# Kernel tuning notes

Hardware: AMD Instinct MI355X
Metric: run time of the kernel (lower is better)

## Reference

```python
import jax, jax.numpy as jnp
import numpy as np

K = 3
PAD = 1
KK = K * K
GROUPS = 32  # min(32, dim) with dim=64
EPS = 1e-5


def _conv(x, w, pad):
    return jax.lax.conv_general_dilated(
        x, w, (1, 1), [(pad, pad), (pad, pad)],
        dimension_numbers=('NCHW', 'OIHW', 'NCHW'))


def _bilinear_gather(x, py, px):
    # x: (B,C,H,W); py,px: (B,KK,H,W) float sampling coords (zero pad outside)
    B, C, H, W = x.shape
    xf = x.reshape(B, C, H * W)
    y0f = jnp.floor(py)
    x0f = jnp.floor(px)
    wy1 = py - y0f  # fractional weights (differentiable path to offsets)
    wx1 = px - x0f
    y0 = y0f.astype(jnp.int32)
    x0 = x0f.astype(jnp.int32)

    def g(yi, xi):
        valid = (yi >= 0) & (yi < H) & (xi >= 0) & (xi < W)
        idx = (jnp.clip(yi, 0, H - 1) * W + jnp.clip(xi, 0, W - 1)).reshape(B, 1, -1)
        v = jnp.take_along_axis(xf, idx, axis=2).reshape(B, C, KK, H, W)
        return v * valid[:, None].astype(x.dtype)

    v00 = g(y0, x0)
    v01 = g(y0, x0 + 1)
    v10 = g(y0 + 1, x0)
    v11 = g(y0 + 1, x0 + 1)
    wy1e = wy1[:, None]
    wx1e = wx1[:, None]
    return (v00 * (1 - wy1e) * (1 - wx1e) + v01 * (1 - wy1e) * wx1e
            + v10 * wy1e * (1 - wx1e) + v11 * wy1e * wx1e)


def _forward(x, w_off1, w_off2, w_mask1, w_mask2, weight, bias, gamma, beta):
    B, C, H, W = x.shape
    # offset branch: 1x1 conv then KxK conv -> (B, 2*KK, H, W)
    off = _conv(_conv(x, w_off1, 0), w_off2, PAD).reshape(B, KK, 2, H, W)
    # mask branch -> sigmoid modulation (B, KK, H, W)
    mask = jax.nn.sigmoid(_conv(_conv(x, w_mask1, 0), w_mask2, PAD))
    # base kernel grid (torchvision deform_conv2d: pairs are (dy, dx) per tap)
    ky = jnp.repeat(jnp.arange(K) - PAD, K).astype(x.dtype)
    kx = jnp.tile(jnp.arange(K) - PAD, K).astype(x.dtype)
    py = off[:, :, 0] + jnp.arange(H, dtype=x.dtype)[None, None, :, None] + ky[None, :, None, None]
    px = off[:, :, 1] + jnp.arange(W, dtype=x.dtype)[None, None, None, :] + kx[None, :, None, None]
    samp = _bilinear_gather(x, py, px)  # (B, C, KK, H, W)
    # depthwise deformable conv: per-channel weight over KK taps, modulated by mask
    out = jnp.einsum('bkhw,ck,bckhw->bchw', mask, weight.reshape(C, KK), samp)
    out = out + bias[None, :, None, None]
    # GroupNorm(32, C)
    g = out.reshape(B, GROUPS, C // GROUPS, H, W)
    mu = g.mean(axis=(2, 3, 4), keepdims=True)
    var = g.var(axis=(2, 3, 4), keepdims=True)
    gn = ((g - mu) * jax.lax.rsqrt(var + EPS)).reshape(B, C, H, W)
    gn = gn * gamma[None, :, None, None] + beta[None, :, None, None]
    return jax.nn.gelu(gn, approximate=False)


def setup_inputs() -> dict:
    key = jax.random.key(0)
    ks = jax.random.split(key, 6)
    B, C, H, W = 4, 64, 128, 128
    x = jax.random.normal(ks[0], (B, C, H, W), dtype=jnp.float32)
    w_off1 = jax.random.normal(ks[1], (C, C, 1, 1), dtype=jnp.float32) * 0.05
    w_off2 = jax.random.normal(ks[2], (2 * KK, C, K, K), dtype=jnp.float32) * 0.02
    w_mask1 = jax.random.normal(ks[3], (C, C, 1, 1), dtype=jnp.float32) * 0.05
    w_mask2 = jax.random.normal(ks[4], (KK, C, K, K), dtype=jnp.float32) * 0.05
    bound = 1.0 / np.sqrt(KK)  # kaiming_uniform(a=1) for (C,1,K,K) -> fan_in=KK
    weight = jax.random.uniform(ks[5], (C, 1, K, K), dtype=jnp.float32,
                                minval=-bound, maxval=bound)
    bias = jnp.zeros((C,), dtype=jnp.float32)
    gamma = jnp.ones((C,), dtype=jnp.float32)
    beta = jnp.zeros((C,), dtype=jnp.float32)
    return {'x': x, 'w_off1': w_off1, 'w_off2': w_off2, 'w_mask1': w_mask1,
            'w_mask2': w_mask2, 'weight': weight, 'bias': bias,
            'gamma': gamma, 'beta': beta}


def reference(x, w_off1, w_off2, w_mask1, w_mask2, weight, bias, gamma, beta):
    return _forward(x, w_off1, w_off2, w_mask1, w_mask2, weight, bias, gamma, beta)
```

## Files before the change

### kernel.cpp

```cpp
#include <hip/hip_runtime.h>
#include <math.h>

#define B_  4
#define C_  64
#define H_  128
#define W_  128
#define HW_ (H_*W_)
#define NPIX_ (B_*HW_)
#define GROUPS_ 32

typedef __attribute__((ext_vector_type(8))) short short8;
typedef __attribute__((ext_vector_type(4))) float f32x4;

__device__ inline short f2bf_rne(float f) {
    unsigned u = __float_as_uint(f);
    unsigned r = (u + 0x7FFFu + ((u >> 16) & 1u)) >> 16;
    return (short)r;
}
__device__ inline float bf2f(short h) {
    return __uint_as_float(((unsigned)(unsigned short)h) << 16);
}

__global__ void k0_prep(const float* __restrict__ w_off1, const float* __restrict__ w_mask1,
                        const float* __restrict__ w_off2, const float* __restrict__ w_mask2,
                        short* __restrict__ w1_hi, short* __restrict__ w1_lo,
                        short* __restrict__ wo_hi, short* __restrict__ wo_lo,
                        short* __restrict__ wm_hi, short* __restrict__ wm_lo) {
    int i = blockIdx.x * 256 + threadIdx.x;
    if (i < 8192) {
        int co = i >> 6, ci = i & 63;
        float v = (co < 64) ? w_off1[co * 64 + ci] : w_mask1[(co - 64) * 64 + ci];
        short h = f2bf_rne(v);
        w1_hi[i] = h;
        w1_lo[i] = f2bf_rne(v - bf2f(h));
    }
    if (i < 32 * 576) {
        int cout = i / 576, r = i % 576;
        int pos = r >> 6, ci = r & 63;
        float v = (cout < 18) ? w_off2[(cout * 64 + ci) * 9 + pos] : 0.f;
        short h = f2bf_rne(v);
        wo_hi[i] = h;
        wo_lo[i] = f2bf_rne(v - bf2f(h));
    }
    if (i < 16 * 576) {
        int cout = i / 576, r = i % 576;
        int pos = r >> 6, ci = r & 63;
        float v = (cout < 9) ? w_mask2[(cout * 64 + ci) * 9 + pos] : 0.f;
        short h = f2bf_rne(v);
        wm_hi[i] = h;
        wm_lo[i] = f2bf_rne(v - bf2f(h));
    }
}

__global__ __launch_bounds__(256) void k1_mfma(const float* __restrict__ x,
                                               const short* __restrict__ w1_hi,
                                               const short* __restrict__ w1_lo,
                                               short* __restrict__ t1b,
                                               short* __restrict__ t2b,
                                               short* __restrict__ xtb) {
    int l   = threadIdx.x & 63;
    int wv  = threadIdx.x >> 6;
    int row = l >> 4, col = l & 15;
    int p0  = blockIdx.x * 128 + wv * 32;
    int b   = p0 >> 14;
    int hw  = p0 & (HW_ - 1);
    const float* xb = x + (size_t)b * C_ * HW_ + hw;

    short8 afr[2][2];
#pragma unroll
    for (int mt = 0; mt < 2; mt++) {
        int pl = mt * 16 + col;
#pragma unroll
        for (int kb = 0; kb < 2; kb++) {
            int ci0 = kb * 32 + row * 8;
            float xv[8];
#pragma unroll
            for (int j = 0; j < 8; j++) xv[j] = xb[(ci0 + j) * HW_ + pl];
            short8 a;
#pragma unroll
            for (int j = 0; j < 8; j++) a[j] = f2bf_rne(xv[j]);
            afr[mt][kb] = a;
            union { short8 s; uint4 u; } cv2; cv2.s = a;
            *(uint4*)(xtb + ((size_t)(p0 + pl)) * 64 + ci0) = cv2.u;
        }
    }

    for (int nt = 0; nt < 8; nt++) {
        int co = nt * 16 + col;
        union { uint4 u; short8 s; } cv;
        short8 bh[2], bl[2];
        const short* ph = w1_hi + (size_t)co * 64 + row * 8;
        const short* pl_ = w1_lo + (size_t)co * 64 + row * 8;
        cv.u = *(const uint4*)(ph);        bh[0] = cv.s;
        cv.u = *(const uint4*)(ph + 32);   bh[1] = cv.s;
        cv.u = *(const uint4*)(pl_);       bl[0] = cv.s;
        cv.u = *(const uint4*)(pl_ + 32);  bl[1] = cv.s;
        short* tgt = (co < 64) ? t1b : t2b;
        int c6 = co & 63;
#pragma unroll
        for (int mt = 0; mt < 2; mt++) {
            f32x4 acc = {0.f, 0.f, 0.f, 0.f};
            acc = __builtin_amdgcn_mfma_f32_16x16x32_bf16(afr[mt][0], bh[0], acc, 0, 0, 0);
            acc = __builtin_amdgcn_mfma_f32_16x16x32_bf16(afr[mt][0], bl[0], acc, 0, 0, 0);
            acc = __builtin_amdgcn_mfma_f32_16x16x32_bf16(afr[mt][1], bh[1], acc, 0, 0, 0);
            acc = __builtin_amdgcn_mfma_f32_16x16x32_bf16(afr[mt][1], bl[1], acc, 0, 0, 0);
#pragma unroll
            for (int r = 0; r < 4; r++) {
                int p = p0 + mt * 16 + row * 4 + r;
                tgt[(size_t)p * 64 + c6] = f2bf_rne(acc[r]);
            }
        }
    }
}

__global__ __launch_bounds__(256) void k2_mfma(const short* __restrict__ t1b,
                                               const short* __restrict__ t2b,
                                               const short* __restrict__ wo_hi,
                                               const short* __restrict__ wo_lo,
                                               const short* __restrict__ wm_hi,
                                               const short* __restrict__ wm_lo,
                                               float* __restrict__ offmask) {
    int l   = threadIdx.x & 63;
    int wv  = threadIdx.x >> 6;
    int row = l >> 4, col = l & 15;
    int blk = blockIdx.x;
    int h   = blk & 127;
    int p0  = blk * 128;
    int w0  = wv * 32;

    f32x4 aco[2][2] = {{{0.f,0.f,0.f,0.f},{0.f,0.f,0.f,0.f}},
                       {{0.f,0.f,0.f,0.f},{0.f,0.f,0.f,0.f}}};
    f32x4 acm[2]    = {{0.f,0.f,0.f,0.f},{0.f,0.f,0.f,0.f}};

    for (int kb = 0; kb < 18; kb++) {
        int pos = kb >> 1;
        int dy = pos / 3 - 1, dx = pos % 3 - 1;
        int ci0 = (kb & 1) * 32 + row * 8;
        int koff = pos * 64 + ci0;
        union { uint4 u; short8 s; } cv;
        short8 boh0, boh1, bol0, bol1, bmh, bml;
        cv.u = *(const uint4*)(wo_hi + (size_t)col * 576 + koff);        boh0 = cv.s;
        cv.u = *(const uint4*)(wo_hi + (size_t)(col + 16) * 576 + koff); boh1 = cv.s;
        cv.u = *(const uint4*)(wo_lo + (size_t)col * 576 + koff);        bol0 = cv.s;
        cv.u = *(const uint4*)(wo_lo + (size_t)(col + 16) * 576 + koff); bol1 = cv.s;
        cv.u = *(const uint4*)(wm_hi + (size_t)col * 576 + koff);        bmh  = cv.s;
        cv.u = *(const uint4*)(wm_lo + (size_t)col * 576 + koff);        bml  = cv.s;
#pragma unroll
        for (int mt = 0; mt < 2; mt++) {
            int w = w0 + mt * 16 + col;
            bool valid = ((unsigned)(h + dy) < 128u) && ((unsigned)(w + dx) < 128u);
            int ps = p0 + w + dy * 128 + dx;
            short8 a1 = {0,0,0,0,0,0,0,0};
            short8 a2 = {0,0,0,0,0,0,0,0};
            if (valid) {
                cv.u = *(const uint4*)(t1b + (size_t)ps * 64 + ci0); a1 = cv.s;
                cv.u = *(const uint4*)(t2b + (size_t)ps * 64 + ci0); a2 = cv.s;
            }
            aco[mt][0] = __builtin_amdgcn_mfma_f32_16x16x32_bf16(a1, boh0, aco[mt][0], 0, 0, 0);
            aco[mt][0] = __builtin_amdgcn_mfma_f32_16x16x32_bf16(a1, bol0, aco[mt][0], 0, 0, 0);
            aco[mt][1] = __builtin_amdgcn_mfma_f32_16x16x32_bf16(a1, boh1, aco[mt][1], 0, 0, 0);
            aco[mt][1] = __builtin_amdgcn_mfma_f32_16x16x32_bf16(a1, bol1, aco[mt][1], 0, 0, 0);
            acm[mt]    = __builtin_amdgcn_mfma_f32_16x16x32_bf16(a2, bmh,  acm[mt],    0, 0, 0);
            acm[mt]    = __builtin_amdgcn_mfma_f32_16x16x32_bf16(a2, bml,  acm[mt],    0, 0, 0);
        }
    }

#pragma unroll
    for (int mt = 0; mt < 2; mt++) {
#pragma unroll
        for (int r = 0; r < 4; r++) {
            int p = p0 + w0 + mt * 16 + row * 4 + r;
            float* om = offmask + (size_t)p * 32;
            om[col] = aco[mt][0][r];
            if (col < 2) om[16 + col] = aco[mt][1][r];
            if (col < 9) om[18 + col] = 1.f / (1.f + expf(-acm[mt][r]));
        }
    }
}

__global__ __launch_bounds__(256) void k3_deform(const short* __restrict__ xtb,
                                                 const float* __restrict__ offmask,
                                                 const float* __restrict__ weight,
                                                 const float* __restrict__ bias,
                                                 float* __restrict__ out_pre) {
    __shared__ float wl[C_ * 9];
    __shared__ float bl[C_];
    for (int i = threadIdx.x; i < C_ * 9; i += 256) wl[i] = weight[i];
    if (threadIdx.x < C_) bl[threadIdx.x] = bias[threadIdx.x];
    __syncthreads();

    int blk   = blockIdx.x;
    int xcd   = blk & 7;
    int slot  = blk >> 3;
    int b     = slot >> 5;
    int r     = (slot & 31) >> 1;
    int hrow  = slot & 1;
    int h     = xcd * 16 + r;
    int pl    = threadIdx.x >> 2;
    int chunk = threadIdx.x & 3;
    int c0    = chunk * 16;
    int w     = hrow * 64 + pl;
    int hw    = h * W_ + w;
    int P     = b * HW_ + hw;

    float acc[16];
#pragma unroll
    for (int i = 0; i < 16; i++) acc[i] = 0.f;

    const float* po = offmask + (size_t)P * 32;
    const short* xb = xtb + (size_t)b * HW_ * 64;

    for (int k = 0; k < 9; k++) {
        float offy = po[2 * k];
        float offx = po[2 * k + 1];
        float mk   = po[18 + k];
        float py = offy + (float)h + (float)(k / 3 - 1);
        float px = offx + (float)w + (float)(k % 3 - 1);
        float y0f = floorf(py), x0f = floorf(px);
        int y0 = (int)y0f, x0 = (int)x0f;
        int y1 = y0 + 1,   x1 = x0 + 1;
        float wy1 = py - y0f, wx1 = px - x0f;
        float wy0 = 1.f - wy1, wx0 = 1.f - wx1;
        bool vy0 = ((unsigned)y0 < (unsigned)H_);
        bool vy1 = ((unsigned)y1 < (unsigned)H_);
        bool vx0 = ((unsigned)x0 < (unsigned)W_);
        bool vx1 = ((unsigned)x1 < (unsigned)W_);
        int cy0 = min(max(y0, 0), H_ - 1);
        int cy1 = min(max(y1, 0), H_ - 1);
        int cx0 = min(max(x0, 0), W_ - 1);
        int cx1 = min(max(x1, 0), W_ - 1);
        float b00 = wy0 * wx0 * ((vy0 && vx0) ? mk : 0.f);
        float b01 = wy0 * wx1 * ((vy0 && vx1) ? mk : 0.f);
        float b10 = wy1 * wx0 * ((vy1 && vx0) ? mk : 0.f);
        float b11 = wy1 * wx1 * ((vy1 && vx1) ? mk : 0.f);

        const short* p00 = xb + ((size_t)cy0 * W_ + cx0) * 64 + c0;
        const short* p01 = xb + ((size_t)cy0 * W_ + cx1) * 64 + c0;
        const short* p10 = xb + ((size_t)cy1 * W_ + cx0) * 64 + c0;
        const short* p11 = xb + ((size_t)cy1 * W_ + cx1) * 64 + c0;

#pragma unroll
        for (int half = 0; half < 2; half++) {
            uint4 u00 = *(const uint4*)(p00 + 8 * half);
            uint4 u01 = *(const uint4*)(p01 + 8 * half);
            uint4 u10 = *(const uint4*)(p10 + 8 * half);
            uint4 u11 = *(const uint4*)(p11 + 8 * half);
            unsigned a00[4] = {u00.x, u00.y, u00.z, u00.w};
            unsigned a01[4] = {u01.x, u01.y, u01.z, u01.w};
            unsigned a10[4] = {u10.x, u10.y, u10.z, u10.w};
            unsigned a11[4] = {u11.x, u11.y, u11.z, u11.w};
#pragma unroll
            for (int d = 0; d < 4; d++) {
                float s_lo = b00 * __uint_as_float(a00[d] << 16)
                           + b01 * __uint_as_float(a01[d] << 16)
                           + b10 * __uint_as_float(a10[d] << 16)
                           + b11 * __uint_as_float(a11[d] << 16);
                float s_hi = b00 * __uint_as_float(a00[d] & 0xFFFF0000u)
                           + b01 * __uint_as_float(a01[d] & 0xFFFF0000u)
                           + b10 * __uint_as_float(a10[d] & 0xFFFF0000u)
                           + b11 * __uint_as_float(a11[d] & 0xFFFF0000u);
                int c = 8 * half + 2 * d;
                acc[c]     += wl[(c0 + c) * 9 + k] * s_lo;
                acc[c + 1] += wl[(c0 + c + 1) * 9 + k] * s_hi;
            }
        }
    }

    float* op = out_pre + ((size_t)b * C_ + c0) * HW_ + hw;
#pragma unroll
    for (int c = 0; c < 16; c++) op[c * HW_] = acc[c] + bl[c0 + c];
}

__global__ __launch_bounds__(1024) void k4_stats(const float* __restrict__ out_pre,
                                                 float* __restrict__ stats) {
    int bg = blockIdx.x;
    const float4* p = (const float4*)(out_pre + (size_t)bg * 2 * HW_);
    float s = 0.f, ss = 0.f;
    for (int i = threadIdx.x; i < 2 * HW_ / 4; i += 1024) {
        float4 v = p[i];
        s  += v.x + v.y + v.z + v.w;
        ss += v.x * v.x + v.y * v.y + v.z * v.z + v.w * v.w;
    }
#pragma unroll
    for (int m = 1; m < 64; m <<= 1) {
        s  += __shfl_xor(s, m);
        ss += __shfl_xor(ss, m);
    }
    __shared__ float ls[32];
    int lane = threadIdx.x & 63, wid = threadIdx.x >> 6;
    if (lane == 0) { ls[wid] = s; ls[16 + wid] = ss; }
    __syncthreads();
    if (threadIdx.x == 0) {
        float S = 0.f, SS = 0.f;
#pragma unroll
        for (int i = 0; i < 16; i++) { S += ls[i]; SS += ls[16 + i]; }
        const float inv = 1.f / (2.f * HW_);
        float mean = S * inv;
        float var  = SS * inv - mean * mean;
        stats[bg * 2]     = mean;
        stats[bg * 2 + 1] = rsqrtf(var + 1e-5f);
    }
}

__global__ __launch_bounds__(256) void k5_norm_gelu(const float* __restrict__ out_pre,
                                                    const float* __restrict__ stats,
                                                    const float* __restrict__ gamma,
                                                    const float* __restrict__ beta,
                                                    float* __restrict__ out) {
    int i = blockIdx.x * 256 + threadIdx.x;
    int e = i << 2;
    int c = (e >> 14) & (C_ - 1);
    int b = e >> 20;
    int bg = b * GROUPS_ + (c >> 1);
    float mean = stats[bg * 2];
    float rstd = stats[bg * 2 + 1];
    float ga = gamma[c] * rstd;
    float be = beta[c] - mean * ga;
    float4 v = ((const float4*)out_pre)[i];
    float4 r;
    float t;
    t = v.x * ga + be; r.x = 0.5f * t * (1.f + erff(t * 0.70710678118654752f));
    t = v.y * ga + be; r.y = 0.5f * t * (1.f + erff(t * 0.70710678118654752f));
    t = v.z * ga + be; r.z = 0.5f * t * (1.f + erff(t * 0.70710678118654752f));
    t = v.w * ga + be; r.w = 0.5f * t * (1.f + erff(t * 0.70710678118654752f));
    ((float4*)out)[i] = r;
}

extern "C" void kernel_launch(void* const* d_in, const int* in_sizes, int n_in,
                              void* d_out, int out_size, void* d_ws, size_t ws_size,
                              hipStream_t stream) {
    const float* x       = (const float*)d_in[0];
    const float* w_off1  = (const float*)d_in[1];
    const float* w_off2  = (const float*)d_in[2];
    const float* w_mask1 = (const float*)d_in[3];
    const float* w_mask2 = (const float*)d_in[4];
    const float* weight  = (const float*)d_in[5];
    const float* bias    = (const float*)d_in[6];
    const float* gamma   = (const float*)d_in[7];
    const float* beta    = (const float*)d_in[8];
    float* out = (float*)d_out;

    char* ws = (char*)d_ws;
    size_t o = 0;
    short* w1_hi = (short*)(ws + o); o += 8192 * 2;
    short* w1_lo = (short*)(ws + o); o += 8192 * 2;
    short* wo_hi = (short*)(ws + o); o += 32 * 576 * 2;
    short* wo_lo = (short*)(ws + o); o += 32 * 576 * 2;
    short* wm_hi = (short*)(ws + o); o += 16 * 576 * 2;
    short* wm_lo = (short*)(ws + o); o += 16 * 576 * 2;
    o = (o + 255) & ~(size_t)255;
    short* t1b     = (short*)(ws + o); o += (size_t)NPIX_ * 64 * 2;
    short* t2b     = (short*)(ws + o); o += (size_t)NPIX_ * 64 * 2;
    short* xtb     = (short*)(ws + o); o += (size_t)NPIX_ * 64 * 2;
    float* offmask = (float*)(ws + o); o += (size_t)NPIX_ * 32 * 4;
    float* out_pre = (float*)(ws + o); o += (size_t)NPIX_ * 64 * 4;
    float* stats   = (float*)(ws + o); o += 256 * 4;

    hipLaunchKernelGGL(k0_prep, dim3(72), dim3(256), 0, stream,
                       w_off1, w_mask1, w_off2, w_mask2,
                       w1_hi, w1_lo, wo_hi, wo_lo, wm_hi, wm_lo);
    hipLaunchKernelGGL(k1_mfma, dim3(NPIX_ / 128), dim3(256), 0, stream,
                       x, w1_hi, w1_lo, t1b, t2b, xtb);
    hipLaunchKernelGGL(k2_mfma, dim3(NPIX_ / 128), dim3(256), 0, stream,
                       t1b, t2b, wo_hi, wo_lo, wm_hi, wm_lo, offmask);
    hipLaunchKernelGGL(k3_deform, dim3(NPIX_ / 64), dim3(256), 0, stream,
                       xtb, offmask, weight, bias, out_pre);
    hipLaunchKernelGGL(k4_stats, dim3(B_ * GROUPS_), dim3(1024), 0, stream,
                       out_pre, stats);
    hipLaunchKernelGGL(k5_norm_gelu, dim3(NPIX_ * 64 / 4 / 256), dim3(256), 0, stream,
                       out_pre, stats, gamma, beta, out);
}
```

Baseline: 169.3 us.

## Fold 1x1 convs into 3x3 conv weights and drop intermediate tensors

The 1x1 offset and mask convolutions are composed algebraically with the following 3x3 convolutions in the prep kernel, producing one combined 32-output 3x3 weight set applied directly to the bf16-transposed input. This removes the t1b/t2b intermediate tensors, the 1x1 MFMA pass and their global memory traffic. The k1 kernel becomes a pure transpose, and k2 software-prefetches the next K-step's weights and activations and uses a launch-bounds occupancy hint. The change alters rounding, since the intermediate is no longer quantised to bf16, and makes the prep kernel do a serial 64-term dot product per weight.

```diff
diff --git a/kernel.cpp b/kernel.cpp
--- a/kernel.cpp
+++ b/kernel.cpp
@@ -20,160 +20,140 @@
 __device__ inline float bf2f(short h) {
     return __uint_as_float(((unsigned)(unsigned short)h) << 16);
 }
+__device__ inline short8 ld8(const short* p) {
+    union { uint4 u; short8 s; } c;
+    c.u = *(const uint4*)p;
+    return c.s;
+}
 
 __global__ void k0_prep(const float* __restrict__ w_off1, const float* __restrict__ w_mask1,
                         const float* __restrict__ w_off2, const float* __restrict__ w_mask2,
-                        short* __restrict__ w1_hi, short* __restrict__ w1_lo,
-                        short* __restrict__ wo_hi, short* __restrict__ wo_lo,
-                        short* __restrict__ wm_hi, short* __restrict__ wm_lo) {
+                        short* __restrict__ wc_hi, short* __restrict__ wc_lo) {
     int i = blockIdx.x * 256 + threadIdx.x;
-    if (i < 8192) {
-        int co = i >> 6, ci = i & 63;
-        float v = (co < 64) ? w_off1[co * 64 + ci] : w_mask1[(co - 64) * 64 + ci];
-        short h = f2bf_rne(v);
-        w1_hi[i] = h;
-        w1_lo[i] = f2bf_rne(v - bf2f(h));
-    }
-    if (i < 32 * 576) {
-        int cout = i / 576, r = i % 576;
-        int pos = r >> 6, ci = r & 63;
-        float v = (cout < 18) ? w_off2[(cout * 64 + ci) * 9 + pos] : 0.f;
-        short h = f2bf_rne(v);
-        wo_hi[i] = h;
-        wo_lo[i] = f2bf_rne(v - bf2f(h));
-    }
-    if (i < 16 * 576) {
-        int cout = i / 576, r = i % 576;
-        int pos = r >> 6, ci = r & 63;
-        float v = (cout < 9) ? w_mask2[(cout * 64 + ci) * 9 + pos] : 0.f;
-        short h = f2bf_rne(v);
-        wm_hi[i] = h;
-        wm_lo[i] = f2bf_rne(v - bf2f(h));
-    }
-}
-
-__global__ __launch_bounds__(256) void k1_mfma(const float* __restrict__ x,
-                                               const short* __restrict__ w1_hi,
-                                               const short* __restrict__ w1_lo,
-                                               short* __restrict__ t1b,
-                                               short* __restrict__ t2b,
-                                               short* __restrict__ xtb) {
+    if (i >= 32 * 576) return;
+    int cout = i / 576;
+    int r    = i % 576;
+    int pos  = r >> 6, ci = r & 63;
+    float s = 0.f;
+    if (cout < 18) {
+        for (int cm = 0; cm < 64; cm++)
+            s += w_off2[(cout * 64 + cm) * 9 + pos] * w_off1[cm * 64 + ci];
+    } else if (cout < 27) {
+        for (int cm = 0; cm < 64; cm++)
+            s += w_mask2[((cout - 18) * 64 + cm) * 9 + pos] * w_mask1[cm * 64 + ci];
+    }
+    short h = f2bf_rne(s);
+    wc_hi[i] = h;
+    wc_lo[i] = f2bf_rne(s - bf2f(h));
+}
+
+__global__ __launch_bounds__(256) void k1_trans(const float* __restrict__ x,
+                                                short* __restrict__ xtb) {
     int l   = threadIdx.x & 63;
     int wv  = threadIdx.x >> 6;
     int row = l >> 4, col = l & 15;
-    int p0  = blockIdx.x * 128 + wv * 32;
+    int p0  = blockIdx.x * 64 + wv * 16;
     int b   = p0 >> 14;
     int hw  = p0 & (HW_ - 1);
     const float* xb = x + (size_t)b * C_ * HW_ + hw;
-
-    short8 afr[2][2];
-#pragma unroll
-    for (int mt = 0; mt < 2; mt++) {
-        int pl = mt * 16 + col;
-#pragma unroll
-        for (int kb = 0; kb < 2; kb++) {
-            int ci0 = kb * 32 + row * 8;
-            float xv[8];
-#pragma unroll
-            for (int j = 0; j < 8; j++) xv[j] = xb[(ci0 + j) * HW_ + pl];
-            short8 a;
-#pragma unroll
-            for (int j = 0; j < 8; j++) a[j] = f2bf_rne(xv[j]);
-            afr[mt][kb] = a;
-            union { short8 s; uint4 u; } cv2; cv2.s = a;
-            *(uint4*)(xtb + ((size_t)(p0 + pl)) * 64 + ci0) = cv2.u;
-        }
-    }
-
-    for (int nt = 0; nt < 8; nt++) {
-        int co = nt * 16 + col;
-        union { uint4 u; short8 s; } cv;
-        short8 bh[2], bl[2];
-        const short* ph = w1_hi + (size_t)co * 64 + row * 8;
-        const short* pl_ = w1_lo + (size_t)co * 64 + row * 8;
-        cv.u = *(const uint4*)(ph);        bh[0] = cv.s;
-        cv.u = *(const uint4*)(ph + 32);   bh[1] = cv.s;
-        cv.u = *(const uint4*)(pl_);       bl[0] = cv.s;
-        cv.u = *(const uint4*)(pl_ + 32);  bl[1] = cv.s;
-        short* tgt = (co < 64) ? t1b : t2b;
-        int c6 = co & 63;
-#pragma unroll
-        for (int mt = 0; mt < 2; mt++) {
-            f32x4 acc = {0.f, 0.f, 0.f, 0.f};
-            acc = __builtin_amdgcn_mfma_f32_16x16x32_bf16(afr[mt][0], bh[0], acc, 0, 0, 0);
-            acc = __builtin_amdgcn_mfma_f32_16x16x32_bf16(afr[mt][0], bl[0], acc, 0, 0, 0);
-            acc = __builtin_amdgcn_mfma_f32_16x16x32_bf16(afr[mt][1], bh[1], acc, 0, 0, 0);
-            acc = __builtin_amdgcn_mfma_f32_16x16x32_bf16(afr[mt][1], bl[1], acc, 0, 0, 0);
-#pragma unroll
-            for (int r = 0; r < 4; r++) {
-                int p = p0 + mt * 16 + row * 4 + r;
-                tgt[(size_t)p * 64 + c6] = f2bf_rne(acc[r]);
-            }
-        }
-    }
-}
-
-__global__ __launch_bounds__(256) void k2_mfma(const short* __restrict__ t1b,
-                                               const short* __restrict__ t2b,
-                                               const short* __restrict__ wo_hi,
-                                               const short* __restrict__ wo_lo,
-                                               const short* __restrict__ wm_hi,
-                                               const short* __restrict__ wm_lo,
-                                               float* __restrict__ offmask) {
+#pragma unroll
+    for (int kb = 0; kb < 2; kb++) {
+        int ci0 = kb * 32 + row * 8;
+        float xv[8];
+#pragma unroll
+        for (int j = 0; j < 8; j++) xv[j] = xb[(ci0 + j) * HW_ + col];
+        short8 a;
+#pragma unroll
+        for (int j = 0; j < 8; j++) a[j] = f2bf_rne(xv[j]);
+        union { short8 s; uint4 u; } cv; cv.s = a;
+        *(uint4*)(xtb + ((size_t)(p0 + col)) * 64 + ci0) = cv.u;
+    }
+}
+
+__global__ __launch_bounds__(256, 2) void k2_mfma(const short* __restrict__ xtb,
+                                                  const short* __restrict__ wc_hi,
+                                                  const short* __restrict__ wc_lo,
+                                                  float* __restrict__ offmask) {
     int l   = threadIdx.x & 63;
     int wv  = threadIdx.x >> 6;
     int row = l >> 4, col = l & 15;
     int blk = blockIdx.x;
     int h   = blk & 127;
-    int p0  = blk * 128;
-    int w0  = wv * 32;
-
-    f32x4 aco[2][2] = {{{0.f,0.f,0.f,0.f},{0.f,0.f,0.f,0.f}},
-                       {{0.f,0.f,0.f,0.f},{0.f,0.f,0.f,0.f}}};
-    f32x4 acm[2]    = {{0.f,0.f,0.f,0.f},{0.f,0.f,0.f,0.f}};
-
-    for (int kb = 0; kb < 18; kb++) {
-        int pos = kb >> 1;
-        int dy = pos / 3 - 1, dx = pos % 3 - 1;
+    int pb  = blk * 128 + wv * 32;
+    int w0  = (pb & 127);
+
+    const short8 zero = {0,0,0,0,0,0,0,0};
+    f32x4 a00 = {0.f,0.f,0.f,0.f};
+    f32x4 a01 = {0.f,0.f,0.f,0.f};
+    f32x4 a10 = {0.f,0.f,0.f,0.f};
+    f32x4 a11 = {0.f,0.f,0.f,0.f};
+
+    short8 cw0, cw1, cw2, cw3, ca0, ca1;
+    {
+        const int kb = 0, pos = 0, dy = -1, dx = -1;
         int ci0 = (kb & 1) * 32 + row * 8;
-        int koff = pos * 64 + ci0;
-        union { uint4 u; short8 s; } cv;
-        short8 boh0, boh1, bol0, bol1, bmh, bml;
-        cv.u = *(const uint4*)(wo_hi + (size_t)col * 576 + koff);        boh0 = cv.s;
-        cv.u = *(const uint4*)(wo_hi + (size_t)(col + 16) * 576 + koff); boh1 = cv.s;
-        cv.u = *(const uint4*)(wo_lo + (size_t)col * 576 + koff);        bol0 = cv.s;
-        cv.u = *(const uint4*)(wo_lo + (size_t)(col + 16) * 576 + koff); bol1 = cv.s;
-        cv.u = *(const uint4*)(wm_hi + (size_t)col * 576 + koff);        bmh  = cv.s;
-        cv.u = *(const uint4*)(wm_lo + (size_t)col * 576 + koff);        bml  = cv.s;
+        int ko  = pos * 64 + ci0;
+        cw0 = ld8(wc_hi + (size_t)col * 576 + ko);
+        cw1 = ld8(wc_lo + (size_t)col * 576 + ko);
+        cw2 = ld8(wc_hi + (size_t)(col + 16) * 576 + ko);
+        cw3 = ld8(wc_lo + (size_t)(col + 16) * 576 + ko);
 #pragma unroll
         for (int mt = 0; mt < 2; mt++) {
+            int pbase = pb + mt * 16 + col;
             int w = w0 + mt * 16 + col;
             bool valid = ((unsigned)(h + dy) < 128u) && ((unsigned)(w + dx) < 128u);
-            int ps = p0 + w + dy * 128 + dx;
-            short8 a1 = {0,0,0,0,0,0,0,0};
-            short8 a2 = {0,0,0,0,0,0,0,0};
-            if (valid) {
-                cv.u = *(const uint4*)(t1b + (size_t)ps * 64 + ci0); a1 = cv.s;
-                cv.u = *(const uint4*)(t2b + (size_t)ps * 64 + ci0); a2 = cv.s;
+            int addr = valid ? (pbase + dy * 128 + dx) : pbase;
+            short8 v = ld8(xtb + (size_t)addr * 64 + ci0);
+            if (mt == 0) ca0 = valid ? v : zero; else ca1 = valid ? v : zero;
+        }
+    }
+
+#pragma unroll
+    for (int kb = 0; kb < 18; kb++) {
+        short8 nw0, nw1, nw2, nw3, na0, na1;
+        if (kb < 17) {
+            const int kn = kb + 1;
+            const int pos = kn >> 1;
+            const int dy = pos / 3 - 1, dx = pos % 3 - 1;
+            int ci0 = (kn & 1) * 32 + row * 8;
+            int ko  = pos * 64 + ci0;
+            nw0 = ld8(wc_hi + (size_t)col * 576 + ko);
+            nw1 = ld8(wc_lo + (size_t)col * 576 + ko);
+            nw2 = ld8(wc_hi + (size_t)(col + 16) * 576 + ko);
+            nw3 = ld8(wc_lo + (size_t)(col + 16) * 576 + ko);
+#pragma unroll
+            for (int mt = 0; mt < 2; mt++) {
+                int pbase = pb + mt * 16 + col;
+                int w = w0 + mt * 16 + col;
+                bool valid = ((unsigned)(h + dy) < 128u) && ((unsigned)(w + dx) < 128u);
+                int addr = valid ? (pbase + dy * 128 + dx) : pbase;
+                short8 v = ld8(xtb + (size_t)addr * 64 + ci0);
+                if (mt == 0) na0 = valid ? v : zero; else na1 = valid ? v : zero;
             }
-            aco[mt][0] = __builtin_amdgcn_mfma_f32_16x16x32_bf16(a1, boh0, aco[mt][0], 0, 0, 0);
-            aco[mt][0] = __builtin_amdgcn_mfma_f32_16x16x32_bf16(a1, bol0, aco[mt][0], 0, 0, 0);
-            aco[mt][1] = __builtin_amdgcn_mfma_f32_16x16x32_bf16(a1, boh1, aco[mt][1], 0, 0, 0);
-            aco[mt][1] = __builtin_amdgcn_mfma_f32_16x16x32_bf16(a1, bol1, aco[mt][1], 0, 0, 0);
-            acm[mt]    = __builtin_amdgcn_mfma_f32_16x16x32_bf16(a2, bmh,  acm[mt],    0, 0, 0);
-            acm[mt]    = __builtin_amdgcn_mfma_f32_16x16x32_bf16(a2, bml,  acm[mt],    0, 0, 0);
         }
+        a00 = __builtin_amdgcn_mfma_f32_16x16x32_bf16(ca0, cw0, a00, 0, 0, 0);
+        a00 = __builtin_amdgcn_mfma_f32_16x16x32_bf16(ca0, cw1, a00, 0, 0, 0);
+        a01 = __builtin_amdgcn_mfma_f32_16x16x32_bf16(ca0, cw2, a01, 0, 0, 0);
+        a01 = __builtin_amdgcn_mfma_f32_16x16x32_bf16(ca0, cw3, a01, 0, 0, 0);
+        a10 = __builtin_amdgcn_mfma_f32_16x16x32_bf16(ca1, cw0, a10, 0, 0, 0);
+        a10 = __builtin_amdgcn_mfma_f32_16x16x32_bf16(ca1, cw1, a10, 0, 0, 0);
+        a11 = __builtin_amdgcn_mfma_f32_16x16x32_bf16(ca1, cw2, a11, 0, 0, 0);
+        a11 = __builtin_amdgcn_mfma_f32_16x16x32_bf16(ca1, cw3, a11, 0, 0, 0);
+        cw0 = nw0; cw1 = nw1; cw2 = nw2; cw3 = nw3;
+        ca0 = na0; ca1 = na1;
     }
 
 #pragma unroll
     for (int mt = 0; mt < 2; mt++) {
+        f32x4 n0 = mt ? a10 : a00;
+        f32x4 n1 = mt ? a11 : a01;
 #pragma unroll
         for (int r = 0; r < 4; r++) {
-            int p = p0 + w0 + mt * 16 + row * 4 + r;
+            int p = pb + mt * 16 + row * 4 + r;
             float* om = offmask + (size_t)p * 32;
-            om[col] = aco[mt][0][r];
-            if (col < 2) om[16 + col] = aco[mt][1][r];
-            if (col < 9) om[18 + col] = 1.f / (1.f + expf(-acm[mt][r]));
+            om[col] = n0[r];
+            if (col < 2)       om[16 + col] = n1[r];
+            else if (col < 11) om[16 + col] = 1.f / (1.f + expf(-n1[r]));
         }
     }
 }
@@ -342,27 +322,20 @@
 
     char* ws = (char*)d_ws;
     size_t o = 0;
-    short* w1_hi = (short*)(ws + o); o += 8192 * 2;
-    short* w1_lo = (short*)(ws + o); o += 8192 * 2;
-    short* wo_hi = (short*)(ws + o); o += 32 * 576 * 2;
-    short* wo_lo = (short*)(ws + o); o += 32 * 576 * 2;
-    short* wm_hi = (short*)(ws + o); o += 16 * 576 * 2;
-    short* wm_lo = (short*)(ws + o); o += 16 * 576 * 2;
+    short* wc_hi = (short*)(ws + o); o += 32 * 576 * 2;
+    short* wc_lo = (short*)(ws + o); o += 32 * 576 * 2;
     o = (o + 255) & ~(size_t)255;
-    short* t1b     = (short*)(ws + o); o += (size_t)NPIX_ * 64 * 2;
-    short* t2b     = (short*)(ws + o); o += (size_t)NPIX_ * 64 * 2;
     short* xtb     = (short*)(ws + o); o += (size_t)NPIX_ * 64 * 2;
     float* offmask = (float*)(ws + o); o += (size_t)NPIX_ * 32 * 4;
     float* out_pre = (float*)(ws + o); o += (size_t)NPIX_ * 64 * 4;
     float* stats   = (float*)(ws + o); o += 256 * 4;
 
     hipLaunchKernelGGL(k0_prep, dim3(72), dim3(256), 0, stream,
-                       w_off1, w_mask1, w_off2, w_mask2,
-                       w1_hi, w1_lo, wo_hi, wo_lo, wm_hi, wm_lo);
-    hipLaunchKernelGGL(k1_mfma, dim3(NPIX_ / 128), dim3(256), 0, stream,
-                       x, w1_hi, w1_lo, t1b, t2b, xtb);
+                       w_off1, w_mask1, w_off2, w_mask2, wc_hi, wc_lo);
+    hipLaunchKernelGGL(k1_trans, dim3(NPIX_ / 64), dim3(256), 0, stream,
+                       x, xtb);
     hipLaunchKernelGGL(k2_mfma, dim3(NPIX_ / 128), dim3(256), 0, stream,
-                       t1b, t2b, wo_hi, wo_lo, wm_hi, wm_lo, offmask);
+                       xtb, wc_hi, wc_lo, offmask);
     hipLaunchKernelGGL(k3_deform, dim3(NPIX_ / 64), dim3(256), 0, stream,
                        xtb, offmask, weight, bias, out_pre);
     hipLaunchKernelGGL(k4_stats, dim3(B_ * GROUPS_), dim3(1024), 0, stream,
```

New measurement: 149.4 us. 11.7% less time.
